# Kernel optimization log

Measured on AMD Instinct MI355X. Metric: run time of the kernel, lower is better.

The kernel has to match this reference:

```python
import jax, jax.numpy as jnp
import numpy as np

V, E, H, L, T, B, K = 50000, 256, 512, 2, 256, 64, 32


def setup_inputs() -> dict:
    key = jax.random.key(0)
    ks = iter(jax.random.split(key, 64))
    def p(shape, scale=0.05):
        return jax.random.normal(next(ks), shape, jnp.float32) * scale
    inp = {"sentences": jax.random.randint(next(ks), (T, B), 0, V)}
    inp["emb"] = p((V, E), 0.1)
    in_sizes = [E, 2 * H]
    for l in range(L):
        for d in ("f", "r"):
            inp[f"w_ih_l{l}{d}"] = p((4 * H, in_sizes[l]))
            inp[f"w_hh_l{l}{d}"] = p((4 * H, H))
            inp[f"b_ih_l{l}{d}"] = p((4 * H,))
            inp[f"b_hh_l{l}{d}"] = p((4 * H,))
    inp["W_out"] = p((K, 2 * H))
    inp["b_out"] = p((K,))
    inp["transitions"] = p((K, K), 0.1)
    inp["start_trans"] = p((K,), 0.1)
    inp["stop_trans"] = p((K,), 0.1)
    return inp


def _lstm_dir(x, w_ih, w_hh, b_ih, b_hh, reverse):
    # x: (T, B, D). PyTorch gate order: i, f, g, o.
    Hd = w_hh.shape[1]
    xp = jnp.einsum('tbd,gd->tbg', x, w_ih) + b_ih + b_hh  # precompute input proj
    def step(carry, xt):
        h, c = carry
        g = xt + h @ w_hh.T
        i, f, gg, o = jnp.split(g, 4, axis=-1)
        c = jax.nn.sigmoid(f) * c + jax.nn.sigmoid(i) * jnp.tanh(gg)
        h = jax.nn.sigmoid(o) * jnp.tanh(c)
        return (h, c), h
    z = jnp.zeros((x.shape[1], Hd), x.dtype)
    _, hs = jax.lax.scan(step, (z, z), xp, reverse=reverse)
    return hs


def _forward(sentences, emb, layer_params, W_out, b_out, transitions, start_trans, stop_trans):
    x = emb[sentences]  # (T, B, E); dropout is identity at inference
    for (pf, pr) in layer_params:
        hf = _lstm_dir(x, *pf, reverse=False)
        hr = _lstm_dir(x, *pr, reverse=True)
        x = jnp.concatenate([hf, hr], axis=-1)  # (T, B, 2H)
    feats = jnp.einsum('tbh,kh->tbk', x, W_out) + b_out  # (T, B, K)

    # Viterbi: R[b, j, k] = transitions[j, k] + dp[b, k] + feat[b, j]
    dp0 = start_trans + feats[0]
    def vstep(dp, feat):
        R = transitions[None] + dp[:, None, :] + feat[:, :, None]
        return R.max(-1), R.argmax(-1)
    dp, bps = jax.lax.scan(vstep, dp0, feats[1:])  # bps: (T-1, B, K)
    dp = dp + stop_trans
    scores = dp.max(-1)
    last = dp.argmax(-1)
    def back(tag, bp_t):
        prev = jnp.take_along_axis(bp_t, tag[:, None], axis=1)[:, 0]
        return prev, prev
    _, pre = jax.lax.scan(back, last, bps, reverse=True)  # (T-1, B), in time order
    paths = jnp.concatenate([pre, last[None]], axis=0)  # (T, B)
    return scores, paths


def reference(sentences, emb,
              w_ih_l0f, w_hh_l0f, b_ih_l0f, b_hh_l0f,
              w_ih_l0r, w_hh_l0r, b_ih_l0r, b_hh_l0r,
              w_ih_l1f, w_hh_l1f, b_ih_l1f, b_hh_l1f,
              w_ih_l1r, w_hh_l1r, b_ih_l1r, b_hh_l1r,
              W_out, b_out, transitions, start_trans, stop_trans):
    layer_params = [
        ((w_ih_l0f, w_hh_l0f, b_ih_l0f, b_hh_l0f), (w_ih_l0r, w_hh_l0r, b_ih_l0r, b_hh_l0r)),
        ((w_ih_l1f, w_hh_l1f, b_ih_l1f, b_hh_l1f), (w_ih_l1r, w_hh_l1r, b_ih_l1r, b_hh_l1r)),
    ]
    return _forward(sentences, emb, layer_params, W_out, b_out, transitions, start_trans, stop_trans)
```

## Files before the change

kernel.cpp:

```cpp
#include <hip/hip_runtime.h>
#include <cstdint>
#include <cstddef>

#define T_ 256
#define B_ 64
#define E_ 256
#define H_ 512
#define NTAG 32
#define CHK 32
#define HSLOT 33

static constexpr size_t OX1  = 0;
static constexpr size_t SX1  = (size_t)T_*256*B_*4;
static constexpr size_t OX2  = OX1 + SX1;
static constexpr size_t SX2  = SX1;
static constexpr size_t OX0  = OX2;
static constexpr size_t OXP  = OX2 + SX2;
static constexpr size_t SXPC = (size_t)CHK*2048*B_;
static constexpr size_t SXP  = 2*SXPC;
static constexpr size_t OWHH0 = OXP + SXP;
static constexpr size_t SWHH  = (size_t)2*512*512*4;
static constexpr size_t OWHH1 = OWHH0 + SWHH;
static constexpr size_t OWIH0 = OWHH1 + SWHH;
static constexpr size_t SWIH0 = (size_t)2*2048*256;
static constexpr size_t OWIH1 = OWIH0 + SWIH0;
static constexpr size_t SWIH1 = (size_t)2*2048*1024;
static constexpr size_t OWOUT = OWIH1 + SWIH1;
static constexpr size_t SWOUT = (size_t)1024*32;
static constexpr size_t OHH   = OWOUT + SWOUT;
static constexpr size_t SHHL  = (size_t)2*HSLOT*32768;
static constexpr size_t SHH   = 2*SHHL;
static constexpr size_t OCB   = OHH + SHH;
static constexpr size_t SCB   = (size_t)2*2*512*64;
static constexpr size_t OBAR  = OCB + SCB;
static constexpr size_t SBAR  = (size_t)2*2*128*16;
static constexpr size_t OFE   = OBAR + SBAR;
static constexpr size_t SFE   = (size_t)T_*B_*NTAG;
static constexpr size_t OBP   = OFE + SFE;
static constexpr size_t SBP   = (size_t)T_*B_*NTAG/4;
static constexpr size_t WS_FLOATS = OBP + SBP;

__device__ __forceinline__ float sigf(float x){ return 1.0f/(1.0f + expf(-x)); }

__global__ void pack_whh(const float* __restrict__ w, float* __restrict__ out){
  int id = blockIdx.x*256 + threadIdx.x;
  int gate = id & 3, k = (id>>2) & 511, u = id >> 11;
  out[id] = w[((size_t)gate*512 + u)*512 + k];
}
__global__ void pack_wih(const float* __restrict__ w, float* __restrict__ out, int K, int kshift){
  int id = blockIdx.x*256 + threadIdx.x;
  int k = id & (K-1); int jj = (id>>kshift)&15; int g = id>>(kshift+4);
  out[((size_t)g*K + k)*16 + jj] = w[(size_t)(g*16+jj)*K + k];
}
__global__ void pack_wout(const float* __restrict__ w, float* __restrict__ out){
  int id = blockIdx.x*256 + threadIdx.x;
  int k = id & 1023, jj = id>>10;
  out[k*32 + jj] = w[id];
}

__global__ void gather_emb(const int* __restrict__ sent, const float* __restrict__ emb,
                           float* __restrict__ x0){
  int t = blockIdx.x; int lane = threadIdx.x & 63; int w = threadIdx.x >> 6;
  int s = sent[t*B_ + lane];
  const float4* er = (const float4*)emb + (size_t)s*(E_/4);
  float4* xo = (float4*)x0 + (size_t)t*64*64;
  #pragma unroll
  for (int q=0; q<16; ++q){
    int e4 = w*16 + q;
    xo[e4*64 + lane] = er[e4];
  }
}

__global__ __launch_bounds__(256) void proj_kernel(
    const float* __restrict__ xin, const float* __restrict__ wpack,
    const float* __restrict__ bihf, const float* __restrict__ bhhf,
    const float* __restrict__ bihr, const float* __restrict__ bhhr,
    float* __restrict__ xp, int K, int t0){
  int jg = blockIdx.x, i = blockIdx.y, dir = blockIdx.z;
  int t = dir ? (T_-1 - (t0 + i)) : (t0 + i);
  int lane = threadIdx.x & 63;
  int w = __builtin_amdgcn_readfirstlane((int)threadIdx.x) >> 6;
  int kq = K >> 2;
  int n4 = kq >> 2;
  int k40 = (w*kq) >> 2;
  const float4* xi = (const float4*)xin + (size_t)t*(K>>2)*64;
  size_t pstride = (size_t)K*16;
  const float* wp = wpack + (size_t)dir*2048*K + (size_t)(jg*2)*pstride + (size_t)w*kq*16;
  float acc[2][16];
  #pragma unroll
  for (int p=0;p<2;p++)
    #pragma unroll
    for (int jj=0;jj<16;jj++) acc[p][jj] = 0.f;
  for (int k4=0; k4<n4; ++k4){
    float4 h = xi[(k40+k4)*64 + lane];
    float hv[4] = {h.x, h.y, h.z, h.w};
    #pragma unroll
    for (int p=0;p<2;p++){
      const float* wv = wp + p*pstride + k4*64;
      #pragma unroll
      for (int ii=0;ii<4;ii++)
        #pragma unroll
        for (int jj=0;jj<16;jj++)
          acc[p][jj] = fmaf(wv[ii*16+jj], hv[ii], acc[p][jj]);
    }
  }
  __shared__ float red[4][32][64];
  #pragma unroll
  for (int p=0;p<2;p++)
    #pragma unroll
    for (int jj=0;jj<16;jj++) red[w][p*16+jj][lane] = acc[p][jj];
  __syncthreads();
  const float* b1 = dir ? bihr : bihf;
  const float* b2 = dir ? bhhr : bhhf;
  float* xpd = xp + (size_t)dir*SXPC + (size_t)i*2048*64;
  #pragma unroll
  for (int q=0;q<8;q++){
    int rr = w*8 + q;
    float v = red[0][rr][lane] + red[1][rr][lane] + red[2][rr][lane] + red[3][rr][lane];
    int row = jg*32 + rr;
    v += b1[row] + b2[row];
    xpd[(size_t)row*64 + lane] = v;
  }
}

__global__ __launch_bounds__(256,1) void rec_kernel(
    const float* __restrict__ xp, const float* __restrict__ whh,
    float* __restrict__ xout, float* __restrict__ hh, float* __restrict__ cb0,
    int* __restrict__ flags, int step0, int nsteps){
  int bid = blockIdx.x;
  int dir = bid & 1, g = bid >> 1;
  int lane = threadIdx.x & 63;
  int w = __builtin_amdgcn_readfirstlane((int)threadIdx.x >> 6);
  const float* xpd = xp + (size_t)dir*SXPC;
  const float* wbase = whh + (size_t)dir*1048576 + (size_t)g*4*2048;
  float* hhd = hh + (size_t)dir*((size_t)HSLOT*32768);
  float* cb = cb0 + dir*32768;
  int* fl = flags + dir*(128*16);
  __shared__ float red[4][16][64];
  __shared__ float hlds[256];
  int uo = g*4 + w;
  float c = cb[uo*64 + lane];
  size_t xb = ((size_t)uo)*64 + lane;
  float x0v = xpd[xb], x1v = xpd[xb+32768], x2v = xpd[xb+65536], x3v = xpd[xb+98304];
  for (int s=0; s<nsteps; ++s){
    int gstep = step0 + s;
    int t = dir ? (T_-1-gstep) : gstep;
    const float4* hp = (const float4*)(hhd + (size_t)(gstep % HSLOT)*32768);
    float4 hreg[32];
    #pragma unroll
    for (int i=0;i<32;i++) hreg[i] = hp[(w*32+i)*64 + lane];
    float acc[4][4];
    #pragma unroll
    for (int cu=0;cu<4;cu++)
      #pragma unroll
      for (int gt=0;gt<4;gt++) acc[cu][gt]=0.f;
    #pragma unroll
    for (int i=0;i<32;i++){
      float hv[4] = {hreg[i].x, hreg[i].y, hreg[i].z, hreg[i].w};
      #pragma unroll
      for (int cu=0; cu<4; cu++){
        const float4* wr = (const float4*)(wbase + (size_t)cu*2048 + (size_t)(w*128 + i*4)*4);
        #pragma unroll
        for (int kk=0;kk<4;kk++){
          float4 w4 = wr[kk];
          acc[cu][0] = fmaf(w4.x, hv[kk], acc[cu][0]);
          acc[cu][1] = fmaf(w4.y, hv[kk], acc[cu][1]);
          acc[cu][2] = fmaf(w4.z, hv[kk], acc[cu][2]);
          acc[cu][3] = fmaf(w4.w, hv[kk], acc[cu][3]);
        }
      }
    }
    #pragma unroll
    for (int cu=0;cu<4;cu++)
      #pragma unroll
      for (int gt=0;gt<4;gt++) red[w][cu*4+gt][lane] = acc[cu][gt];
    __syncthreads();
    float gv[4];
    #pragma unroll
    for (int gt=0;gt<4;gt++)
      gv[gt] = red[0][w*4+gt][lane] + red[1][w*4+gt][lane]
             + red[2][w*4+gt][lane] + red[3][w*4+gt][lane];
    gv[0] += x0v; gv[1] += x1v; gv[2] += x2v; gv[3] += x3v;
    float iv = sigf(gv[0]), fv = sigf(gv[1]);
    float gg = tanhf(gv[2]), ov = sigf(gv[3]);
    c = fv*c + iv*gg;
    float h = ov*tanhf(c);
    hlds[lane*4 + w] = h;
    __syncthreads();
    if (w == 0){
      float4 hv4 = ((const float4*)hlds)[lane];
      union { float4 f; unsigned long long q[2]; } uu; uu.f = hv4;
      unsigned long long* dst = (unsigned long long*)
          (hhd + (size_t)((gstep+1) % HSLOT)*32768 + (size_t)g*256 + (size_t)lane*4);
      __hip_atomic_store(dst+0, uu.q[0], __ATOMIC_RELAXED, __HIP_MEMORY_SCOPE_AGENT);
      __hip_atomic_store(dst+1, uu.q[1], __ATOMIC_RELAXED, __HIP_MEMORY_SCOPE_AGENT);
    } else if (w == 1){
      float4 hv4 = ((const float4*)hlds)[lane];
      float4* xo = (float4*)(xout + (size_t)t*65536 + (size_t)(dir*128 + g)*256);
      xo[lane] = hv4;
    }
    if (s < nsteps-1){
      if (w == 0){
        asm volatile("s_waitcnt vmcnt(0)" ::: "memory");
      }
      __syncthreads();
      if (threadIdx.x == 0)
        __hip_atomic_store(&fl[g*16], gstep+1, __ATOMIC_RELAXED, __HIP_MEMORY_SCOPE_AGENT);
      size_t xb2 = ((size_t)(s+1)*2048 + uo)*64 + lane;
      x0v = xpd[xb2]; x1v = xpd[xb2+32768]; x2v = xpd[xb2+65536]; x3v = xpd[xb2+98304];
      int tid = threadIdx.x;
      if (tid < 128){
        int target = gstep+1;
        int spins = 0;
        while (__hip_atomic_load(&fl[tid*16], __ATOMIC_RELAXED, __HIP_MEMORY_SCOPE_AGENT) < target){
          __builtin_amdgcn_s_sleep(1);
          if (++spins > (1<<22)) break;
        }
      }
      __syncthreads();
      asm volatile("" ::: "memory");
    }
  }
  cb[uo*64 + lane] = c;
}

__global__ __launch_bounds__(256) void feats_kernel(
    const float* __restrict__ x2, const float* __restrict__ wout,
    const float* __restrict__ bout, float* __restrict__ feats){
  int t = blockIdx.x; int lane = threadIdx.x & 63;
  int w = __builtin_amdgcn_readfirstlane((int)threadIdx.x) >> 6;
  const float4* xi = (const float4*)x2 + (size_t)t*16384;
  const float* wp = wout + (size_t)w*256*32;
  float acc[32];
  #pragma unroll
  for (int j=0;j<32;j++) acc[j] = 0.f;
  for (int k4=0;k4<64;k4++){
    float4 h = xi[(w*64 + k4)*64 + lane];
    float hv[4] = {h.x, h.y, h.z, h.w};
    const float* wv = wp + k4*128;
    #pragma unroll
    for (int ii=0;ii<4;ii++)
      #pragma unroll
      for (int j=0;j<32;j++)
        acc[j] = fmaf(wv[ii*32+j], hv[ii], acc[j]);
  }
  __shared__ float red[4][32][64];
  #pragma unroll
  for (int j=0;j<32;j++) red[w][j][lane] = acc[j];
  __syncthreads();
  __shared__ float tr[64*33];
  #pragma unroll
  for (int q=0;q<8;q++){
    int j = w*8 + q;
    float v = red[0][j][lane]+red[1][j][lane]+red[2][j][lane]+red[3][j][lane] + bout[j];
    tr[lane*33 + j] = v;
  }
  __syncthreads();
  float* fo = feats + (size_t)t*2048;
  int tid = threadIdx.x;
  #pragma unroll
  for (int q=0;q<8;q++){
    int idx = tid*8 + q;
    fo[idx] = tr[(idx>>5)*33 + (idx&31)];
  }
}

__global__ __launch_bounds__(64) void viterbi_kernel(
    const float* __restrict__ feats, const float* __restrict__ trans,
    const float* __restrict__ start, const float* __restrict__ stop,
    unsigned char* __restrict__ bp, float* __restrict__ out){
  int lane = threadIdx.x & 63;
  int b = blockIdx.x*2 + (lane>>5);
  int j = lane & 31;
  int base = lane & 32;
  float tr[32];
  #pragma unroll
  for (int k=0;k<32;k++) tr[k] = trans[j*32+k];
  float dp = start[j] + feats[b*32 + j];
  for (int t=1;t<T_;t++){
    float best = __shfl(dp, base, 64) + tr[0];
    int arg = 0;
    #pragma unroll
    for (int k=1;k<32;k++){
      float v = __shfl(dp, base + k, 64) + tr[k];
      if (v > best){ best = v; arg = k; }
    }
    dp = best + feats[((size_t)t*64 + b)*32 + j];
    bp[(size_t)(t-1)*2048 + b*32 + j] = (unsigned char)arg;
  }
  dp += stop[j];
  float bv = dp; int bi = j;
  #pragma unroll
  for (int off=1; off<32; off<<=1){
    float ov = __shfl_xor(bv, off, 64);
    int oi   = __shfl_xor(bi, off, 64);
    if (ov > bv || (ov == bv && oi < bi)){ bv = ov; bi = oi; }
  }
  if (j == 0){
    out[b] = bv;
    int cur = bi;
    out[64 + 255*64 + b] = (float)cur;
    for (int t=254;t>=0;t--){
      cur = bp[(size_t)t*2048 + b*32 + cur];
      out[64 + t*64 + b] = (float)cur;
    }
  }
}

extern "C" void kernel_launch(void* const* d_in, const int* in_sizes, int n_in,
                              void* d_out, int out_size, void* d_ws, size_t ws_size,
                              hipStream_t stream){
  const int*   sent      = (const int*)  d_in[0];
  const float* emb       = (const float*)d_in[1];
  const float* w_ih_l0f  = (const float*)d_in[2];
  const float* w_hh_l0f  = (const float*)d_in[3];
  const float* b_ih_l0f  = (const float*)d_in[4];
  const float* b_hh_l0f  = (const float*)d_in[5];
  const float* w_ih_l0r  = (const float*)d_in[6];
  const float* w_hh_l0r  = (const float*)d_in[7];
  const float* b_ih_l0r  = (const float*)d_in[8];
  const float* b_hh_l0r  = (const float*)d_in[9];
  const float* w_ih_l1f  = (const float*)d_in[10];
  const float* w_hh_l1f  = (const float*)d_in[11];
  const float* b_ih_l1f  = (const float*)d_in[12];
  const float* b_hh_l1f  = (const float*)d_in[13];
  const float* w_ih_l1r  = (const float*)d_in[14];
  const float* w_hh_l1r  = (const float*)d_in[15];
  const float* b_ih_l1r  = (const float*)d_in[16];
  const float* b_hh_l1r  = (const float*)d_in[17];
  const float* W_out     = (const float*)d_in[18];
  const float* b_out     = (const float*)d_in[19];
  const float* trans     = (const float*)d_in[20];
  const float* start_t   = (const float*)d_in[21];
  const float* stop_t    = (const float*)d_in[22];
  float* ws  = (float*)d_ws;
  float* out = (float*)d_out;

  if (ws_size < WS_FLOATS * sizeof(float)) return;

  hipMemsetAsync(ws + OHH, 0, (SHH + SCB + SBAR)*sizeof(float), stream);

  pack_whh<<<4096,256,0,stream>>>(w_hh_l0f, ws + OWHH0);
  pack_whh<<<4096,256,0,stream>>>(w_hh_l0r, ws + OWHH0 + 1048576);
  pack_whh<<<4096,256,0,stream>>>(w_hh_l1f, ws + OWHH1);
  pack_whh<<<4096,256,0,stream>>>(w_hh_l1r, ws + OWHH1 + 1048576);
  pack_wih<<<2048,256,0,stream>>>(w_ih_l0f, ws + OWIH0,           256, 8);
  pack_wih<<<2048,256,0,stream>>>(w_ih_l0r, ws + OWIH0 + 524288,  256, 8);
  pack_wih<<<8192,256,0,stream>>>(w_ih_l1f, ws + OWIH1,           1024, 10);
  pack_wih<<<8192,256,0,stream>>>(w_ih_l1r, ws + OWIH1 + 2097152, 1024, 10);
  pack_wout<<<128,256,0,stream>>>(W_out, ws + OWOUT);

  gather_emb<<<256,256,0,stream>>>(sent, emb, ws + OX0);

  const int NCH = T_ / CHK;
  dim3 gp(64, CHK, 2);
  int* bar = (int*)(ws + OBAR);

  for (int c = 0; c < NCH; ++c){
    proj_kernel<<<gp,256,0,stream>>>(ws+OX0, ws+OWIH0,
                                     b_ih_l0f,b_hh_l0f,b_ih_l0r,b_hh_l0r,
                                     ws+OXP, 256, c*CHK);
    rec_kernel<<<256,256,0,stream>>>(ws+OXP, ws+OWHH0, ws+OX1,
                                     ws+OHH, ws+OCB, bar, c*CHK, CHK);
  }
  for (int c = 0; c < NCH; ++c){
    proj_kernel<<<gp,256,0,stream>>>(ws+OX1, ws+OWIH1,
                                     b_ih_l1f,b_hh_l1f,b_ih_l1r,b_hh_l1r,
                                     ws+OXP, 1024, c*CHK);
    rec_kernel<<<256,256,0,stream>>>(ws+OXP, ws+OWHH1, ws+OX2,
                                     ws+OHH+SHHL, ws+OCB+65536,
                                     bar + 4096, c*CHK, CHK);
  }
  feats_kernel<<<256,256,0,stream>>>(ws+OX2, ws+OWOUT, b_out, ws+OFE);
  viterbi_kernel<<<32,64,0,stream>>>(ws+OFE, trans, start_t, stop_t,
                                     (unsigned char*)(ws+OBP), out);
}
```

Measured before the change: 8.943 ms.

## Overlap next-chunk input projection with LSTM recurrence in one fused launch

The separate projection and recurrence kernels per chunk are merged into one launch of 512 blocks. Blocks 0-255 run the recurrence at raised priority, and blocks 256+ compute the input projection for the next chunk into a double buffer. This hides projection time behind the latency-bound recurrence and cuts the number of launches. Layer 1 uses a smaller chunk of 16 to fit the buffers. The risk is that projection blocks share CUs with the spinning recurrence blocks (launch bounds now allow 2 per CU) and could slow the critical path.

```diff
diff --git a/kernel.cpp b/kernel.cpp
--- a/kernel.cpp
+++ b/kernel.cpp
@@ -8,16 +8,21 @@
 #define H_ 512
 #define NTAG 32
 #define CHK 32
+#define CHK1 16
 #define HSLOT 33
+#define SPIN_MAX (1<<20)
 
 static constexpr size_t OX1  = 0;
 static constexpr size_t SX1  = (size_t)T_*256*B_*4;
 static constexpr size_t OX2  = OX1 + SX1;
 static constexpr size_t SX2  = SX1;
 static constexpr size_t OX0  = OX2;
+static constexpr size_t SX0  = (size_t)T_*64*B_*4;
 static constexpr size_t OXP  = OX2 + SX2;
-static constexpr size_t SXPC = (size_t)CHK*2048*B_;
-static constexpr size_t SXP  = 2*SXPC;
+static constexpr size_t SXPC0 = (size_t)CHK*2048*B_;
+static constexpr size_t SXPC1 = (size_t)CHK1*2048*B_;
+static constexpr size_t SXP  = 2*SXPC0;
+static constexpr size_t OXPB0 = OX2 + SX0;
 static constexpr size_t OWHH0 = OXP + SXP;
 static constexpr size_t SWHH  = (size_t)2*512*512*4;
 static constexpr size_t OWHH1 = OWHH0 + SWHH;
@@ -75,7 +80,7 @@
     const float* __restrict__ xin, const float* __restrict__ wpack,
     const float* __restrict__ bihf, const float* __restrict__ bhhf,
     const float* __restrict__ bihr, const float* __restrict__ bhhr,
-    float* __restrict__ xp, int K, int t0){
+    float* __restrict__ xp, size_t xp_ds, int K, int t0){
   int jg = blockIdx.x, i = blockIdx.y, dir = blockIdx.z;
   int t = dir ? (T_-1 - (t0 + i)) : (t0 + i);
   int lane = threadIdx.x & 63;
@@ -112,7 +117,7 @@
   __syncthreads();
   const float* b1 = dir ? bihr : bihf;
   const float* b2 = dir ? bhhr : bhhf;
-  float* xpd = xp + (size_t)dir*SXPC + (size_t)i*2048*64;
+  float* xpd = xp + (size_t)dir*xp_ds + (size_t)i*2048*64;
   #pragma unroll
   for (int q=0;q<8;q++){
     int rr = w*8 + q;
@@ -123,21 +128,83 @@
   }
 }
 
-__global__ __launch_bounds__(256,1) void rec_kernel(
-    const float* __restrict__ xp, const float* __restrict__ whh,
+__global__ __launch_bounds__(256,2) void fused_kernel(
+    const float* __restrict__ xpA, const float* __restrict__ whh,
     float* __restrict__ xout, float* __restrict__ hh, float* __restrict__ cb0,
-    int* __restrict__ flags, int step0, int nsteps){
+    int* __restrict__ flags, int step0, int nsteps, size_t xpA_ds,
+    const float* __restrict__ xin, const float* __restrict__ wih,
+    const float* __restrict__ bihf, const float* __restrict__ bhhf,
+    const float* __restrict__ bihr, const float* __restrict__ bhhr,
+    float* __restrict__ xpB, size_t xpB_ds, int projK, int projT0, int projCHK){
+  __shared__ float red[4][16][64];
+  __shared__ float hlds[256];
+  __shared__ float redp[4][32][64];
   int bid = blockIdx.x;
-  int dir = bid & 1, g = bid >> 1;
   int lane = threadIdx.x & 63;
   int w = __builtin_amdgcn_readfirstlane((int)threadIdx.x >> 6);
-  const float* xpd = xp + (size_t)dir*SXPC;
+
+  if (bid >= 256){
+    if (projK == 0) return;
+    int p = bid - 256;
+    int jg = p & 63, r = p >> 6;
+    int tpb = projCHK >> 1;
+    int kq = projK >> 2;
+    int n4 = kq >> 2;
+    int k40 = (w*kq) >> 2;
+    size_t pstride = (size_t)projK*16;
+    for (int q=0; q<tpb; ++q){
+      int idx = r*tpb + q;
+      int dirp = (idx >= projCHK) ? 1 : 0;
+      int i = idx - dirp*projCHK;
+      int t = dirp ? (T_-1 - (projT0 + i)) : (projT0 + i);
+      const float4* xi = (const float4*)xin + (size_t)t*(projK>>2)*64;
+      const float* wp = wih + (size_t)dirp*2048*projK + (size_t)(jg*2)*pstride + (size_t)w*kq*16;
+      float acc[2][16];
+      #pragma unroll
+      for (int pp=0;pp<2;pp++)
+        #pragma unroll
+        for (int jj=0;jj<16;jj++) acc[pp][jj] = 0.f;
+      for (int k4=0; k4<n4; ++k4){
+        float4 h = xi[(k40+k4)*64 + lane];
+        float hv[4] = {h.x, h.y, h.z, h.w};
+        #pragma unroll
+        for (int pp=0;pp<2;pp++){
+          const float* wv = wp + pp*pstride + k4*64;
+          #pragma unroll
+          for (int ii=0;ii<4;ii++)
+            #pragma unroll
+            for (int jj=0;jj<16;jj++)
+              acc[pp][jj] = fmaf(wv[ii*16+jj], hv[ii], acc[pp][jj]);
+        }
+      }
+      #pragma unroll
+      for (int pp=0;pp<2;pp++)
+        #pragma unroll
+        for (int jj=0;jj<16;jj++) redp[w][pp*16+jj][lane] = acc[pp][jj];
+      __syncthreads();
+      const float* b1 = dirp ? bihr : bihf;
+      const float* b2 = dirp ? bhhr : bhhf;
+      float* xpd = xpB + (size_t)dirp*xpB_ds + (size_t)i*2048*64;
+      #pragma unroll
+      for (int q2=0;q2<8;q2++){
+        int rr = w*8 + q2;
+        float v = redp[0][rr][lane] + redp[1][rr][lane] + redp[2][rr][lane] + redp[3][rr][lane];
+        int row = jg*32 + rr;
+        v += b1[row] + b2[row];
+        xpd[(size_t)row*64 + lane] = v;
+      }
+      __syncthreads();
+    }
+    return;
+  }
+
+  __builtin_amdgcn_s_setprio(1);
+  int dir = bid & 1, g = bid >> 1;
+  const float* xpd = xpA + (size_t)dir*xpA_ds;
   const float* wbase = whh + (size_t)dir*1048576 + (size_t)g*4*2048;
   float* hhd = hh + (size_t)dir*((size_t)HSLOT*32768);
   float* cb = cb0 + dir*32768;
   int* fl = flags + dir*(128*16);
-  __shared__ float red[4][16][64];
-  __shared__ float hlds[256];
   int uo = g*4 + w;
   float c = cb[uo*64 + lane];
   size_t xb = ((size_t)uo)*64 + lane;
@@ -189,11 +256,11 @@
     __syncthreads();
     if (w == 0){
       float4 hv4 = ((const float4*)hlds)[lane];
-      union { float4 f; unsigned long long q[2]; } uu; uu.f = hv4;
+      union { float4 f; unsigned long long qq[2]; } uu; uu.f = hv4;
       unsigned long long* dst = (unsigned long long*)
           (hhd + (size_t)((gstep+1) % HSLOT)*32768 + (size_t)g*256 + (size_t)lane*4);
-      __hip_atomic_store(dst+0, uu.q[0], __ATOMIC_RELAXED, __HIP_MEMORY_SCOPE_AGENT);
-      __hip_atomic_store(dst+1, uu.q[1], __ATOMIC_RELAXED, __HIP_MEMORY_SCOPE_AGENT);
+      __hip_atomic_store(dst+0, uu.qq[0], __ATOMIC_RELAXED, __HIP_MEMORY_SCOPE_AGENT);
+      __hip_atomic_store(dst+1, uu.qq[1], __ATOMIC_RELAXED, __HIP_MEMORY_SCOPE_AGENT);
     } else if (w == 1){
       float4 hv4 = ((const float4*)hlds)[lane];
       float4* xo = (float4*)(xout + (size_t)t*65536 + (size_t)(dir*128 + g)*256);
@@ -214,7 +281,7 @@
         int spins = 0;
         while (__hip_atomic_load(&fl[tid*16], __ATOMIC_RELAXED, __HIP_MEMORY_SCOPE_AGENT) < target){
           __builtin_amdgcn_s_sleep(1);
-          if (++spins > (1<<22)) break;
+          if (++spins > SPIN_MAX) break;
         }
       }
       __syncthreads();
@@ -352,24 +419,42 @@
 
   gather_emb<<<256,256,0,stream>>>(sent, emb, ws + OX0);
 
-  const int NCH = T_ / CHK;
-  dim3 gp(64, CHK, 2);
   int* bar = (int*)(ws + OBAR);
 
-  for (int c = 0; c < NCH; ++c){
+  {
+    float* bufA = ws + OXP;
+    float* bufB = ws + OXPB0;
+    dim3 gp(64, CHK, 2);
     proj_kernel<<<gp,256,0,stream>>>(ws+OX0, ws+OWIH0,
                                      b_ih_l0f,b_hh_l0f,b_ih_l0r,b_hh_l0r,
-                                     ws+OXP, 256, c*CHK);
-    rec_kernel<<<256,256,0,stream>>>(ws+OXP, ws+OWHH0, ws+OX1,
-                                     ws+OHH, ws+OCB, bar, c*CHK, CHK);
-  }
-  for (int c = 0; c < NCH; ++c){
+                                     bufA, SXPC0, 256, 0);
+    const int NCH = T_ / CHK;
+    for (int c = 0; c < NCH; ++c){
+      int projK = (c < NCH-1) ? 256 : 0;
+      fused_kernel<<<512,256,0,stream>>>(
+          bufA, ws+OWHH0, ws+OX1, ws+OHH, ws+OCB, bar, c*CHK, CHK, SXPC0,
+          ws+OX0, ws+OWIH0, b_ih_l0f,b_hh_l0f,b_ih_l0r,b_hh_l0r,
+          bufB, SXPC0, projK, (c+1)*CHK, CHK);
+      float* tmp = bufA; bufA = bufB; bufB = tmp;
+    }
+  }
+  {
+    float* bufA = ws + OXP;
+    float* bufB = ws + OXP + 2*SXPC1;
+    dim3 gp(64, CHK1, 2);
     proj_kernel<<<gp,256,0,stream>>>(ws+OX1, ws+OWIH1,
                                      b_ih_l1f,b_hh_l1f,b_ih_l1r,b_hh_l1r,
-                                     ws+OXP, 1024, c*CHK);
-    rec_kernel<<<256,256,0,stream>>>(ws+OXP, ws+OWHH1, ws+OX2,
-                                     ws+OHH+SHHL, ws+OCB+65536,
-                                     bar + 4096, c*CHK, CHK);
+                                     bufA, SXPC1, 1024, 0);
+    const int NCH = T_ / CHK1;
+    for (int c = 0; c < NCH; ++c){
+      int projK = (c < NCH-1) ? 1024 : 0;
+      fused_kernel<<<512,256,0,stream>>>(
+          bufA, ws+OWHH1, ws+OX2, ws+OHH+SHHL, ws+OCB+65536, bar+4096,
+          c*CHK1, CHK1, SXPC1,
+          ws+OX1, ws+OWIH1, b_ih_l1f,b_hh_l1f,b_ih_l1r,b_hh_l1r,
+          bufB, SXPC1, projK, (c+1)*CHK1, CHK1);
+      float* tmp = bufA; bufA = bufB; bufB = tmp;
+    }
   }
   feats_kernel<<<256,256,0,stream>>>(ws+OX2, ws+OWOUT, b_out, ws+OFE);
   viterbi_kernel<<<32,64,0,stream>>>(ws+OFE, trans, start_t, stop_t,
```

Measured after the change: 13.72 ms. 1.53x slower.

## Overlap next-chunk input projection with recurrent steps inside rec_kernel

Applied to the files above, without the earlier changes.

Moves the input projection for the next time chunk into the recurrent kernel. Each wave does a bounded slice of projection work while it waits at the per-step spin barrier, and results go to double-buffered xp arrays. Layer 1 uses a smaller chunk of 16 steps, and only the first chunk keeps a standalone proj_kernel launch. The aim is to fill barrier idle time and cut the serial proj/rec launches. In exchange it adds register pressure and latency to the critical recurrent step; the feats kernel also switches to float4 weight loads.

```diff
diff --git a/kernel.cpp b/kernel.cpp
--- a/kernel.cpp
+++ b/kernel.cpp
@@ -8,6 +8,7 @@
 #define H_ 512
 #define NTAG 32
 #define CHK 32
+#define CHK1 16
 #define HSLOT 33
 
 static constexpr size_t OX1  = 0;
@@ -15,9 +16,12 @@
 static constexpr size_t OX2  = OX1 + SX1;
 static constexpr size_t SX2  = SX1;
 static constexpr size_t OX0  = OX2;
+static constexpr size_t SX0  = (size_t)T_*64*B_*4;
 static constexpr size_t OXP  = OX2 + SX2;
-static constexpr size_t SXPC = (size_t)CHK*2048*B_;
-static constexpr size_t SXP  = 2*SXPC;
+static constexpr size_t SXPC0 = (size_t)CHK*2048*B_;
+static constexpr size_t SXPC1 = (size_t)CHK1*2048*B_;
+static constexpr size_t SXP  = 2*SXPC0;
+static constexpr size_t OXPB0 = OX2 + SX0;
 static constexpr size_t OWHH0 = OXP + SXP;
 static constexpr size_t SWHH  = (size_t)2*512*512*4;
 static constexpr size_t OWHH1 = OWHH0 + SWHH;
@@ -75,7 +79,7 @@
     const float* __restrict__ xin, const float* __restrict__ wpack,
     const float* __restrict__ bihf, const float* __restrict__ bhhf,
     const float* __restrict__ bihr, const float* __restrict__ bhhr,
-    float* __restrict__ xp, int K, int t0){
+    float* __restrict__ xp, size_t xp_ds, int K, int t0){
   int jg = blockIdx.x, i = blockIdx.y, dir = blockIdx.z;
   int t = dir ? (T_-1 - (t0 + i)) : (t0 + i);
   int lane = threadIdx.x & 63;
@@ -112,7 +116,7 @@
   __syncthreads();
   const float* b1 = dir ? bihr : bihf;
   const float* b2 = dir ? bhhr : bhhf;
-  float* xpd = xp + (size_t)dir*SXPC + (size_t)i*2048*64;
+  float* xpd = xp + (size_t)dir*xp_ds + (size_t)i*2048*64;
   #pragma unroll
   for (int q=0;q<8;q++){
     int rr = w*8 + q;
@@ -123,15 +127,81 @@
   }
 }
 
+__device__ __forceinline__ void proj_run(
+    int budget, int& ppass, int& ppos, float (&pacc)[2][16],
+    int pc0, int pg2, int pniter, int projNP, int projCHK, int projK, int projT0,
+    const float* __restrict__ pxin, const float* __restrict__ pwih,
+    const float* __restrict__ pbihf, const float* __restrict__ pbhhf,
+    const float* __restrict__ pbihr, const float* __restrict__ pbhhr,
+    float* __restrict__ pxp, size_t pxp_ds, int lane){
+  while (budget > 0 && ppass < projNP){
+    int cb0 = pc0 + 16*ppass;
+    int dirp = (cb0 >= projCHK) ? 1 : 0;
+    int ibase = cb0 - dirp*projCHK;
+    int ti0 = dirp ? (T_-1-(projT0+ibase))   : (projT0+ibase);
+    int ti1 = dirp ? (T_-1-(projT0+ibase+8)) : (projT0+ibase+8);
+    const float4* px0 = (const float4*)pxin + (size_t)ti0*(projK>>2)*64;
+    const float4* px1 = (const float4*)pxin + (size_t)ti1*(projK>>2)*64;
+    const float4* pw4 = (const float4*)(pwih + (size_t)dirp*2048*projK
+                                             + (size_t)pg2*projK*16);
+    int todo = pniter - ppos;
+    int run = todo < budget ? todo : budget;
+    for (int z=0; z<run; ++z){
+      float4 ha = px0[(size_t)ppos*64 + lane];
+      float4 hb = px1[(size_t)ppos*64 + lane];
+      float ha_[4] = {ha.x, ha.y, ha.z, ha.w};
+      float hb_[4] = {hb.x, hb.y, hb.z, hb.w};
+      const float4* wv = pw4 + (size_t)ppos*16;
+      #pragma unroll
+      for (int kk=0; kk<4; ++kk){
+        #pragma unroll
+        for (int r=0; r<4; ++r){
+          float4 w4 = wv[kk*4 + r];
+          pacc[0][r*4+0] = fmaf(w4.x, ha_[kk], pacc[0][r*4+0]);
+          pacc[0][r*4+1] = fmaf(w4.y, ha_[kk], pacc[0][r*4+1]);
+          pacc[0][r*4+2] = fmaf(w4.z, ha_[kk], pacc[0][r*4+2]);
+          pacc[0][r*4+3] = fmaf(w4.w, ha_[kk], pacc[0][r*4+3]);
+          pacc[1][r*4+0] = fmaf(w4.x, hb_[kk], pacc[1][r*4+0]);
+          pacc[1][r*4+1] = fmaf(w4.y, hb_[kk], pacc[1][r*4+1]);
+          pacc[1][r*4+2] = fmaf(w4.z, hb_[kk], pacc[1][r*4+2]);
+          pacc[1][r*4+3] = fmaf(w4.w, hb_[kk], pacc[1][r*4+3]);
+        }
+      }
+      ppos++;
+    }
+    budget -= run;
+    if (ppos == pniter){
+      const float* b1 = dirp ? pbihr : pbihf;
+      const float* b2 = dirp ? pbhhr : pbhhf;
+      float* pd0 = pxp + (size_t)dirp*pxp_ds + (size_t)ibase*131072;
+      float* pd1 = pd0 + (size_t)8*131072;
+      #pragma unroll
+      for (int jj=0; jj<16; ++jj){
+        int row = pg2*16 + jj;
+        float bs = b1[row] + b2[row];
+        pd0[(size_t)row*64 + lane] = pacc[0][jj] + bs;
+        pd1[(size_t)row*64 + lane] = pacc[1][jj] + bs;
+        pacc[0][jj] = 0.f; pacc[1][jj] = 0.f;
+      }
+      ppass++; ppos = 0;
+    }
+  }
+}
+
 __global__ __launch_bounds__(256,1) void rec_kernel(
     const float* __restrict__ xp, const float* __restrict__ whh,
     float* __restrict__ xout, float* __restrict__ hh, float* __restrict__ cb0,
-    int* __restrict__ flags, int step0, int nsteps){
+    int* __restrict__ flags, int step0, int nsteps, size_t xp_ds,
+    const float* __restrict__ pxin, const float* __restrict__ pwih,
+    const float* __restrict__ pbihf, const float* __restrict__ pbhhf,
+    const float* __restrict__ pbihr, const float* __restrict__ pbhhr,
+    float* __restrict__ pxp, size_t pxp_ds,
+    int projK, int projT0, int projCHK, int projNP, int projIT){
   int bid = blockIdx.x;
   int dir = bid & 1, g = bid >> 1;
   int lane = threadIdx.x & 63;
   int w = __builtin_amdgcn_readfirstlane((int)threadIdx.x >> 6);
-  const float* xpd = xp + (size_t)dir*SXPC;
+  const float* xpd = xp + (size_t)dir*xp_ds;
   const float* wbase = whh + (size_t)dir*1048576 + (size_t)g*4*2048;
   float* hhd = hh + (size_t)dir*((size_t)HSLOT*32768);
   float* cb = cb0 + dir*32768;
@@ -142,6 +212,15 @@
   float c = cb[uo*64 + lane];
   size_t xb = ((size_t)uo)*64 + lane;
   float x0v = xpd[xb], x1v = xpd[xb+32768], x2v = xpd[xb+65536], x3v = xpd[xb+98304];
+  int W = bid*4 + w;
+  int pg2 = W & 127, pc0 = W >> 7;
+  int pniter = projK >> 2;
+  int ppass = 0, ppos = 0;
+  float pacc[2][16];
+  #pragma unroll
+  for (int q=0;q<2;q++)
+    #pragma unroll
+    for (int jj=0;jj<16;jj++) pacc[q][jj] = 0.f;
   for (int s=0; s<nsteps; ++s){
     int gstep = step0 + s;
     int t = dir ? (T_-1-gstep) : gstep;
@@ -208,6 +287,10 @@
         __hip_atomic_store(&fl[g*16], gstep+1, __ATOMIC_RELAXED, __HIP_MEMORY_SCOPE_AGENT);
       size_t xb2 = ((size_t)(s+1)*2048 + uo)*64 + lane;
       x0v = xpd[xb2]; x1v = xpd[xb2+32768]; x2v = xpd[xb2+65536]; x3v = xpd[xb2+98304];
+      if (projK)
+        proj_run(projIT, ppass, ppos, pacc, pc0, pg2, pniter, projNP, projCHK,
+                 projK, projT0, pxin, pwih, pbihf, pbhhf, pbihr, pbhhr,
+                 pxp, pxp_ds, lane);
       int tid = threadIdx.x;
       if (tid < 128){
         int target = gstep+1;
@@ -221,6 +304,10 @@
       asm volatile("" ::: "memory");
     }
   }
+  if (projK)
+    proj_run(0x7fffffff, ppass, ppos, pacc, pc0, pg2, pniter, projNP, projCHK,
+             projK, projT0, pxin, pwih, pbihf, pbhhf, pbihr, pbhhr,
+             pxp, pxp_ds, lane);
   cb[uo*64 + lane] = c;
 }
 
@@ -237,12 +324,18 @@
   for (int k4=0;k4<64;k4++){
     float4 h = xi[(w*64 + k4)*64 + lane];
     float hv[4] = {h.x, h.y, h.z, h.w};
-    const float* wv = wp + k4*128;
-    #pragma unroll
-    for (int ii=0;ii<4;ii++)
-      #pragma unroll
-      for (int j=0;j<32;j++)
-        acc[j] = fmaf(wv[ii*32+j], hv[ii], acc[j]);
+    const float4* wv4 = (const float4*)(wp + k4*128);
+    #pragma unroll
+    for (int ii=0;ii<4;ii++){
+      #pragma unroll
+      for (int q=0;q<8;q++){
+        float4 w4 = wv4[ii*8 + q];
+        acc[q*4+0] = fmaf(w4.x, hv[ii], acc[q*4+0]);
+        acc[q*4+1] = fmaf(w4.y, hv[ii], acc[q*4+1]);
+        acc[q*4+2] = fmaf(w4.z, hv[ii], acc[q*4+2]);
+        acc[q*4+3] = fmaf(w4.w, hv[ii], acc[q*4+3]);
+      }
+    }
   }
   __shared__ float red[4][32][64];
   #pragma unroll
@@ -352,24 +445,40 @@
 
   gather_emb<<<256,256,0,stream>>>(sent, emb, ws + OX0);
 
-  const int NCH = T_ / CHK;
-  dim3 gp(64, CHK, 2);
   int* bar = (int*)(ws + OBAR);
 
-  for (int c = 0; c < NCH; ++c){
-    proj_kernel<<<gp,256,0,stream>>>(ws+OX0, ws+OWIH0,
-                                     b_ih_l0f,b_hh_l0f,b_ih_l0r,b_hh_l0r,
-                                     ws+OXP, 256, c*CHK);
-    rec_kernel<<<256,256,0,stream>>>(ws+OXP, ws+OWHH0, ws+OX1,
-                                     ws+OHH, ws+OCB, bar, c*CHK, CHK);
-  }
-  for (int c = 0; c < NCH; ++c){
-    proj_kernel<<<gp,256,0,stream>>>(ws+OX1, ws+OWIH1,
-                                     b_ih_l1f,b_hh_l1f,b_ih_l1r,b_hh_l1r,
-                                     ws+OXP, 1024, c*CHK);
-    rec_kernel<<<256,256,0,stream>>>(ws+OXP, ws+OWHH1, ws+OX2,
-                                     ws+OHH+SHHL, ws+OCB+65536,
-                                     bar + 4096, c*CHK, CHK);
+  {
+    float* bA = ws + OXP;
+    float* bB = ws + OXPB0;
+    dim3 gp0(64, CHK, 2);
+    proj_kernel<<<gp0,256,0,stream>>>(ws+OX0, ws+OWIH0,
+                                      b_ih_l0f,b_hh_l0f,b_ih_l0r,b_hh_l0r,
+                                      bA, SXPC0, 256, 0);
+    for (int c = 0; c < T_/CHK; ++c){
+      int pk = (c < T_/CHK - 1) ? 256 : 0;
+      rec_kernel<<<256,256,0,stream>>>(
+          bA, ws+OWHH0, ws+OX1, ws+OHH, ws+OCB, bar, c*CHK, CHK, SXPC0,
+          ws+OX0, ws+OWIH0, b_ih_l0f,b_hh_l0f,b_ih_l0r,b_hh_l0r,
+          bB, SXPC0, pk, (c+1)*CHK, CHK, 4, 10);
+      float* tmp = bA; bA = bB; bB = tmp;
+    }
+  }
+  {
+    float* bA = ws + OXP;
+    float* bB = ws + OXP + 2*SXPC1;
+    dim3 gp1(64, CHK1, 2);
+    proj_kernel<<<gp1,256,0,stream>>>(ws+OX1, ws+OWIH1,
+                                      b_ih_l1f,b_hh_l1f,b_ih_l1r,b_hh_l1r,
+                                      bA, SXPC1, 1024, 0);
+    for (int c = 0; c < T_/CHK1; ++c){
+      int pk = (c < T_/CHK1 - 1) ? 1024 : 0;
+      rec_kernel<<<256,256,0,stream>>>(
+          bA, ws+OWHH1, ws+OX2, ws+OHH+SHHL, ws+OCB+65536, bar+4096,
+          c*CHK1, CHK1, SXPC1,
+          ws+OX1, ws+OWIH1, b_ih_l1f,b_hh_l1f,b_ih_l1r,b_hh_l1r,
+          bB, SXPC1, pk, (c+1)*CHK1, CHK1, 2, 36);
+      float* tmp = bA; bA = bB; bB = tmp;
+    }
   }
   feats_kernel<<<256,256,0,stream>>>(ws+OX2, ws+OWOUT, b_out, ws+OFE);
   viterbi_kernel<<<32,64,0,stream>>>(ws+OFE, trans, start_t, stop_t,
```

Measured after the change: 10.58 ms. 1.18x slower.
